# Kernel optimization log

Hardware: AMD Instinct MI355X
Metric: run time of the kernel (lower is better)

Reference implementation:

```python
import jax, jax.numpy as jnp
import numpy as np

N_NODES = 50000
N_EDGES = 1600000
IN_CH = 129   # encoding_dim + node_dim
OUT_CH = 64
PERIODS = 25
N_TRAIN = 25000


def setup_inputs() -> dict:
    key = jax.random.key(0)
    ks = jax.random.split(key, 24)
    inp = {
        'x': jax.random.normal(ks[0], (N_NODES, IN_CH, PERIODS), dtype=jnp.float32),
        'edge_index': jax.random.randint(ks[1], (2, N_EDGES), 0, N_NODES, dtype=jnp.int64),
        'y': jax.random.uniform(ks[2], (N_NODES,), dtype=jnp.float32),
        'train_idx': jax.random.randint(ks[3], (N_TRAIN,), 0, N_NODES, dtype=jnp.int64),
    }
    s_in = 1.0 / np.sqrt(IN_CH)
    s_2o = 1.0 / np.sqrt(2 * OUT_CH)
    s_o = 1.0 / np.sqrt(OUT_CH)
    # TGCN gate params: GCNConv weight/bias (IN_CH->OUT_CH), Linear(2*OUT_CH->OUT_CH)
    names = ['z', 'r', 'h']
    for i, g in enumerate(names):
        inp[f'W_{g}'] = jax.random.uniform(ks[4 + 4 * i], (IN_CH, OUT_CH), minval=-s_in, maxval=s_in)
        inp[f'b_{g}'] = jax.random.uniform(ks[5 + 4 * i], (OUT_CH,), minval=-s_in, maxval=s_in)
        inp[f'Wl_{g}'] = jax.random.uniform(ks[6 + 4 * i], (2 * OUT_CH, OUT_CH), minval=-s_2o, maxval=s_2o)
        inp[f'bl_{g}'] = jax.random.uniform(ks[7 + 4 * i], (OUT_CH,), minval=-s_2o, maxval=s_2o)
    inp['attention'] = jax.random.uniform(ks[16], (PERIODS,), dtype=jnp.float32)
    inp['W_o'] = jax.random.uniform(ks[17], (OUT_CH, 1), minval=-s_o, maxval=s_o)
    inp['b_o'] = jax.random.uniform(ks[18], (1,), minval=-s_o, maxval=s_o)
    return inp


def _forward(x, edge_index, y, train_idx, attention,
             W_z, b_z, Wl_z, bl_z, W_r, b_r, Wl_r, bl_r,
             W_h, b_h, Wl_h, bl_h, W_o, b_o):
    N = x.shape[0]
    src, dst = edge_index[0], edge_index[1]
    # GCN symmetric norm with self-loops (edge_weight = 1)
    deg = 1.0 + jax.ops.segment_sum(jnp.ones_like(src, dtype=x.dtype), dst, num_segments=N)
    dinv = jax.lax.rsqrt(deg)
    edge_norm = (dinv[src] * dinv[dst])[:, None]   # (E,1)
    self_norm = (dinv * dinv)[:, None]              # (N,1)

    def gcn(xt, W, b):
        h = xt @ W                                   # (N, OUT_CH)
        agg = jax.ops.segment_sum(edge_norm * h[src], dst, num_segments=N)
        return agg + self_norm * h + b

    probs = jax.nn.softmax(attention)               # (PERIODS,)
    x_seq = jnp.transpose(x, (2, 0, 1))             # (T, N, IN_CH)

    def step(carry, xp):
        H, acc = carry
        xt, p = xp
        Z = jax.nn.sigmoid(jnp.concatenate([gcn(xt, W_z, b_z), H], axis=1) @ Wl_z + bl_z)
        R = jax.nn.sigmoid(jnp.concatenate([gcn(xt, W_r, b_r), H], axis=1) @ Wl_r + bl_r)
        H_tilde = jnp.tanh(jnp.concatenate([gcn(xt, W_h, b_h), H * R], axis=1) @ Wl_h + bl_h)
        H = Z * H + (1.0 - Z) * H_tilde
        return (H, acc + p * H), None

    H0 = jnp.zeros((N, OUT_CH), dtype=x.dtype)
    (H, H_accum), _ = jax.lax.scan(step, (H0, H0), (x_seq, probs))

    out = jax.nn.sigmoid(H_accum @ W_o + b_o)       # (N, 1)
    y_pred = out[:, 0][train_idx]
    return y_pred, y[train_idx]


def reference(x, edge_index, y, train_idx, attention,
              W_z, b_z, Wl_z, bl_z, W_r, b_r, Wl_r, bl_r,
              W_h, b_h, Wl_h, bl_h, W_o, b_o):
    return _forward(x, edge_index, y, train_idx, attention,
                    W_z, b_z, Wl_z, bl_z, W_r, b_r, Wl_r, bl_r,
                    W_h, b_h, Wl_h, bl_h, W_o, b_o)
```

## Files before the change

### kernel.cpp

```cpp
#include <hip/hip_runtime.h>
#include <stdint.h>

#define NND 50000
#define NNDP 50016
#define NE  1600000
#define INC 129
#define TP  25
#define NTR 25000
#define MPAD 50048
#define NB_SCAN 196
#define CSR_MAX (NE + 8*NND + 128)
#define NFRAG 92
#define WLDS_BYTES (NFRAG*1024)

typedef short bf16x8 __attribute__((ext_vector_type(8)));
typedef float f32x4 __attribute__((ext_vector_type(4)));
typedef float f32x2 __attribute__((ext_vector_type(2)));
typedef uint32_t u32x4 __attribute__((ext_vector_type(4)));

__device__ __forceinline__ uint32_t f2bf(float f){
  union{float ff; uint32_t u;} v; v.ff=f;
  return (v.u + 0x7FFFu + ((v.u>>16)&1u))>>16;
}
__device__ __forceinline__ uint32_t pack2(float a, float b){
  return f2bf(a) | (f2bf(b)<<16);
}
__device__ __forceinline__ float sigm(float v){ return 1.f/(1.f+__expf(-v)); }

__global__ void k_prep(const float* Wz, const float* bz, const float* Wlz, const float* blz,
                       const float* Wr, const float* br, const float* Wlr, const float* blr,
                       const float* Wh, const float* bh, const float* Wlh, const float* blh,
                       uint16_t* WfT, uint16_t* Wlf)
{
  int idx = blockIdx.x*256 + threadIdx.x;
  if (idx < 192*224) {
    int j = idx / 224, k = idx - j*224;
    int g = j >> 6, jj = j & 63;
    const float* W  = g==0?Wz :(g==1?Wr :Wh);
    const float* Wl = g==0?Wlz:(g==1?Wlr:Wlh);
    const float* b  = g==0?bz :(g==1?br :bh);
    const float* bl = g==0?blz:(g==1?blr:blh);
    float v = 0.f;
    if (k < INC) {
      for (int m=0;m<64;m++) v += W[k*64+m]*Wl[m*64+jj];
    } else if (k == 129) {
      v = bl[jj];
      for (int m=0;m<64;m++) v += b[m]*Wl[m*64+jj];
    } else if (k >= 160) {
      v = (g<2) ? Wl[(64+(k-160))*64 + jj] : 0.f;
    }
    int rt = jj>>4, c16 = jj&15;
    int kk = k>>5, kgrp = (k>>3)&3, e = k&7;
    int lane = kgrp*16 + c16;
    WfT[((((g*7+kk)*4+rt)*256 + lane*4 + (e>>1))<<1) + (e&1)] = (uint16_t)f2bf(v);
  } else if (idx < 192*224 + 4096) {
    int t2 = idx - 192*224; int j2 = t2>>6, k2 = t2&63;
    float v = Wlh[(64+k2)*64 + j2];
    int rt = j2>>4, c16 = j2&15;
    int kk2 = k2>>5, kgrp = (k2>>3)&3, e = k2&7;
    int lane = kgrp*16 + c16;
    Wlf[(((kk2*4+rt)*256 + lane*4 + (e>>1))<<1) + (e&1)] = (uint16_t)f2bf(v);
  }
}

__global__ void k_probs(const float* att, float* probs){
  if (threadIdx.x==0 && blockIdx.x==0){
    float m=-1e30f;
    for (int i=0;i<TP;i++) m = fmaxf(m, att[i]);
    float e[TP]; float s=0.f;
    for (int i=0;i<TP;i++){ e[i]=__expf(att[i]-m); s+=e[i]; }
    for (int i=0;i<TP;i++) probs[i]=e[i]/s;
  }
}

__global__ void k_hist(const int* eidx, int* deg){
  int e = blockIdx.x*256 + threadIdx.x;
  if (e < NE) atomicAdd(&deg[eidx[NE + e]], 1);
}

__global__ void k_dinv(const int* deg, float* dinv){
  int n = blockIdx.x*256 + threadIdx.x;
  if (n < NND) dinv[n] = rsqrtf(1.0f + (float)deg[n]);
}

__global__ void k_scan1(const int* deg, int* row_ptr, int* bsum){
  __shared__ int s[256];
  int tid = threadIdx.x;
  int i = blockIdx.x*256 + tid;
  int v = (i < NND) ? ((deg[i]+8)&~7) : 0;
  s[tid] = v; __syncthreads();
  for (int d=1; d<256; d<<=1){
    int t = (tid>=d) ? s[tid-d] : 0;
    __syncthreads();
    s[tid] += t; __syncthreads();
  }
  if (i < NND) row_ptr[i] = s[tid] - v;
  if (tid == 255) bsum[blockIdx.x] = s[255];
}
__global__ void k_scan2(int* bsum, int* boff, int* row_ptr){
  __shared__ int s[256];
  int tid = threadIdx.x;
  int v = (tid < NB_SCAN) ? bsum[tid] : 0;
  s[tid] = v; __syncthreads();
  for (int d=1; d<256; d<<=1){
    int t = (tid>=d) ? s[tid-d] : 0;
    __syncthreads();
    s[tid] += t; __syncthreads();
  }
  if (tid < NB_SCAN) boff[tid] = s[tid] - v;
  if (tid == NB_SCAN-1) row_ptr[NND] = s[tid];
}
__global__ void k_scan3(int* row_ptr, const int* boff){
  int i = blockIdx.x*256 + threadIdx.x;
  if (i < NND) row_ptr[i] += boff[blockIdx.x];
}

__global__ void k_fill(const int* eidx, const int* rp, int* cnt, uint16_t* csr){
  int e = blockIdx.x*256 + threadIdx.x;
  if (e < NE){
    int s = eidx[e], d = eidx[NE+e];
    int pos = rp[d] + atomicAdd(&cnt[d],1);
    csr[pos] = (uint16_t)s;
  }
}
__global__ void k_self(const int* rp, const int* deg, uint16_t* csr){
  int n = blockIdx.x*256 + threadIdx.x;
  if (n < NND){
    int base = rp[n] + deg[n];
    int endp = rp[n+1];
    csr[base] = (uint16_t)n;
    for (int j=base+1; j<endp; j++) csr[j] = (uint16_t)NND;
  }
}

__global__ __launch_bounds__(256) void k_transpose3(const float* __restrict__ x,
                                                    const float* __restrict__ dinv,
                                                    uint32_t* __restrict__ xT8,
                                                    float* __restrict__ xsl){
  __shared__ float lx[3232];
  int n = blockIdx.x;
  const float* xr = x + (size_t)n*(INC*TP);
  for (int e=threadIdx.x; e<INC*TP; e+=256) lx[e] = xr[e];
  __syncthreads();
  float dv = dinv[n];
  for (int idx=threadIdx.x; idx<TP*32; idx+=256){
    int t = idx>>5, u = idx&31;
    int c0 = u*4;
    float v0 = lx[(c0+0)*TP+t]*dv, v1 = lx[(c0+1)*TP+t]*dv;
    float v2 = lx[(c0+2)*TP+t]*dv, v3 = lx[(c0+3)*TP+t]*dv;
    int wlo = __builtin_amdgcn_cvt_pk_fp8_f32(v0, v1, 0, false);
    int w   = __builtin_amdgcn_cvt_pk_fp8_f32(v2, v3, wlo, true);
    xT8[((size_t)t*NNDP + n)*32 + u] = (uint32_t)w;
  }
  for (int t=threadIdx.x; t<TP; t+=256)
    xsl[(size_t)t*NNDP + n] = dv*lx[128*TP + t];
  if (blockIdx.x == 0){
    for (int idx=threadIdx.x; idx<TP*32; idx+=256){
      int t = idx>>5, u = idx&31;
      xT8[((size_t)t*NNDP + NND)*32 + u] = 0u;
    }
    for (int t=threadIdx.x; t<TP; t+=256) xsl[(size_t)t*NNDP + NND] = 0.f;
  }
}

__global__ __launch_bounds__(256) void k_agg(const uint16_t* __restrict__ xT8,
    const int* __restrict__ rp, const uint16_t* __restrict__ csr,
    const float* __restrict__ dinv, uint32_t* __restrict__ AX)
{
  int t = blockIdx.y;
  int wave = threadIdx.x>>6, lane = threadIdx.x&63;
  int d = blockIdx.x*4 + wave;
  int beg = __builtin_amdgcn_readfirstlane(rp[d]);
  int end = __builtin_amdgcn_readfirstlane(rp[d+1]);
  const uint16_t* tbl = xT8 + (size_t)t*((size_t)NNDP*64);
  float a0=0.f, a1=0.f;
  for (int i0=beg; i0<end; i0+=8){
    ulonglong2 c = *(const ulonglong2*)(csr + i0);
    #pragma unroll
    for (int k=0;k<4;k++){
      int s0 = (int)((c.x >> (k*16)) & 0xFFFFu);
      int s1 = (int)((c.y >> (k*16)) & 0xFFFFu);
      uint32_t u0 = tbl[(size_t)s0*64 + lane];
      uint32_t u1 = tbl[(size_t)s1*64 + lane];
      f32x2 v0 = __builtin_amdgcn_cvt_pk_f32_fp8((int)u0, false);
      f32x2 v1 = __builtin_amdgcn_cvt_pk_f32_fp8((int)u1, false);
      a0 += v0.x; a1 += v0.y;
      a0 += v1.x; a1 += v1.y;
    }
  }
  float dv = dinv[d];
  AX[(size_t)t*((size_t)MPAD*80) + (size_t)d*80 + lane] = pack2(dv*a0, dv*a1);
}

__global__ void k_aggL(const float* __restrict__ xsl,
    const int* __restrict__ rp, const uint16_t* __restrict__ csr,
    const float* __restrict__ dinv, uint32_t* __restrict__ AX)
{
  int t = blockIdx.y;
  int d = blockIdx.x*256 + threadIdx.x;
  if (d >= NND) return;
  const float* pl = xsl + (size_t)t*NNDP;
  float a = 0.f;
  int beg=rp[d], end=rp[d+1];
  #pragma unroll 4
  for (int i=beg;i<end;i++) a += pl[(int)csr[i]];
  AX[(size_t)t*((size_t)MPAD*80) + (size_t)d*80 + 64] = pack2(dinv[d]*a, 1.0f);
}

__device__ __forceinline__ u32x4 build_frag(uint32_t Pa0, uint32_t Pa1,
                                            uint32_t Pb0, uint32_t Pb1,
                                            int srcA, int srcB, bool rsel){
  uint32_t a0 = (uint32_t)__shfl((int)Pa0, srcA);
  uint32_t b0 = (uint32_t)__shfl((int)Pb0, srcA);
  uint32_t a1 = (uint32_t)__shfl((int)Pa1, srcA);
  uint32_t b1 = (uint32_t)__shfl((int)Pb1, srcA);
  uint32_t a2 = (uint32_t)__shfl((int)Pa0, srcB);
  uint32_t b2 = (uint32_t)__shfl((int)Pb0, srcB);
  uint32_t a3 = (uint32_t)__shfl((int)Pa1, srcB);
  uint32_t b3 = (uint32_t)__shfl((int)Pb1, srcB);
  u32x4 o;
  o.x = rsel?b0:a0; o.y = rsel?b1:a1; o.z = rsel?b2:a2; o.w = rsel?b3:a3;
  return o;
}

__global__ __launch_bounds__(512, 2) void k_gru(const uint32_t* __restrict__ AX,
    const uint32_t* __restrict__ Wall, float* __restrict__ accum,
    const float* __restrict__ probs)
{
  extern __shared__ uint32_t ldsW[];
  int tid = threadIdx.x;
  int lane = tid & 63, wave = tid >> 6;
  int c16 = lane & 15, q = lane >> 4;
  int node = blockIdx.x*128 + wave*16 + c16;
  bool rsel = (q & 2) != 0;
  int srcA = ((2*q)&3)*16 + c16;
  int srcB = ((2*q+1)&3)*16 + c16;

  {
    const u32x4* src = (const u32x4*)Wall;
    u32x4* dst = (u32x4*)ldsW;
    for (int i = tid; i < NFRAG*64; i += 512) dst[i] = src[i];
  }
  __syncthreads();

  f32x4 h[4] = {};
  f32x4 acr[4] = {};
  u32x4 hf0 = {0,0,0,0}, hf1 = {0,0,0,0};

  for (int t=0; t<TP; t++){
    const uint32_t* AXrow = AX + (size_t)t*((size_t)MPAD*80) + (size_t)node*80 + q*4;
    bf16x8 ax0 = __builtin_nontemporal_load((const bf16x8*)(AXrow));
    bf16x8 ax1 = __builtin_nontemporal_load((const bf16x8*)(AXrow+16));
    bf16x8 ax2 = __builtin_nontemporal_load((const bf16x8*)(AXrow+32));
    bf16x8 ax3 = __builtin_nontemporal_load((const bf16x8*)(AXrow+48));
    bf16x8 ax4 = __builtin_nontemporal_load((const bf16x8*)(AXrow+64));

    f32x4 accg[3][4] = {};
    #pragma unroll
    for (int kk=0; kk<7; kk++){
      bf16x8 xv;
      if      (kk==0) xv = ax0;
      else if (kk==1) xv = ax1;
      else if (kk==2) xv = ax2;
      else if (kk==3) xv = ax3;
      else if (kk==4) xv = ax4;
      else if (kk==5) xv = __builtin_bit_cast(bf16x8, hf0);
      else            xv = __builtin_bit_cast(bf16x8, hf1);
      #pragma unroll
      for (int g=0; g<3; g++){
        if (g==2 && kk>=5) continue;
        #pragma unroll
        for (int rt=0; rt<4; rt++){
          bf16x8 wv = *(const bf16x8*)&ldsW[(((g*7+kk)*4+rt)<<8) + lane*4];
          accg[g][rt] = __builtin_amdgcn_mfma_f32_16x16x32_bf16(wv, xv, accg[g][rt],0,0,0);
        }
      }
    }

    uint32_t Phr[4][2];
    #pragma unroll
    for (int rt=0; rt<4; rt++){
      float hrv[4];
      #pragma unroll
      for (int j=0;j<4;j++){
        float z = sigm(accg[0][rt][j]);
        float r = sigm(accg[1][rt][j]);
        accg[0][rt][j] = z;
        hrv[j] = h[rt][j]*r;
      }
      Phr[rt][0] = pack2(hrv[0], hrv[1]);
      Phr[rt][1] = pack2(hrv[2], hrv[3]);
    }
    u32x4 hrf0 = build_frag(Phr[0][0],Phr[0][1],Phr[1][0],Phr[1][1], srcA,srcB,rsel);
    u32x4 hrf1 = build_frag(Phr[2][0],Phr[2][1],Phr[3][0],Phr[3][1], srcA,srcB,rsel);

    f32x4 acc2[4] = {};
    #pragma unroll
    for (int kk2=0; kk2<2; kk2++){
      bf16x8 bv = __builtin_bit_cast(bf16x8, kk2 ? hrf1 : hrf0);
      #pragma unroll
      for (int rt=0; rt<4; rt++){
        bf16x8 wv = *(const bf16x8*)&ldsW[((84+kk2*4+rt)<<8) + lane*4];
        acc2[rt] = __builtin_amdgcn_mfma_f32_16x16x32_bf16(wv, bv, acc2[rt],0,0,0);
      }
    }

    float pt = probs[t];
    uint32_t Ph[4][2];
    #pragma unroll
    for (int rt=0; rt<4; rt++){
      #pragma unroll
      for (int j=0;j<4;j++){
        float ht = tanhf(acc2[rt][j] + accg[2][rt][j]);
        float z  = accg[0][rt][j];
        float hn = z*h[rt][j] + (1.f-z)*ht;
        h[rt][j] = hn;
        acr[rt][j] += pt*hn;
      }
      Ph[rt][0] = pack2(h[rt][0], h[rt][1]);
      Ph[rt][1] = pack2(h[rt][2], h[rt][3]);
    }
    hf0 = build_frag(Ph[0][0],Ph[0][1],Ph[1][0],Ph[1][1], srcA,srcB,rsel);
    hf1 = build_frag(Ph[2][0],Ph[2][1],Ph[3][0],Ph[3][1], srcA,srcB,rsel);
  }

  if (node < NND){
    #pragma unroll
    for (int rt=0; rt<4; rt++)
      *(f32x4*)&accum[(size_t)node*64 + rt*16 + q*4] = acr[rt];
  }
}

__global__ void k_out(const int* train_idx, const float* accum, const float* Wo,
                      const float* bo, const float* y, float* out){
  int i = blockIdx.x*256 + threadIdx.x;
  if (i < NTR){
    int n = train_idx[i];
    float s = bo[0];
    const float* ar = accum + (size_t)n*64;
    #pragma unroll
    for (int j=0;j<64;j++) s += ar[j]*Wo[j];
    out[i] = sigm(s);
    out[NTR+i] = y[n];
  }
}

extern "C" void kernel_launch(void* const* d_in, const int* in_sizes, int n_in,
                              void* d_out, int out_size, void* d_ws, size_t ws_size,
                              hipStream_t stream)
{
  const float* x   = (const float*)d_in[0];
  const int*   eix = (const int*)d_in[1];
  const float* y   = (const float*)d_in[2];
  const int*   tri = (const int*)d_in[3];
  const float* Wz  = (const float*)d_in[4];
  const float* bz  = (const float*)d_in[5];
  const float* Wlz = (const float*)d_in[6];
  const float* blz = (const float*)d_in[7];
  const float* Wr  = (const float*)d_in[8];
  const float* br  = (const float*)d_in[9];
  const float* Wlr = (const float*)d_in[10];
  const float* blr = (const float*)d_in[11];
  const float* Wh  = (const float*)d_in[12];
  const float* bh  = (const float*)d_in[13];
  const float* Wlh = (const float*)d_in[14];
  const float* blh = (const float*)d_in[15];
  const float* att = (const float*)d_in[16];
  const float* Wo  = (const float*)d_in[17];
  const float* bo  = (const float*)d_in[18];
  float* out = (float*)d_out;

  char* w = (char*)d_ws;
  size_t off = 0;
  auto alloc = [&](size_t sz)->size_t{ size_t o=off; off=(off+sz+255)&~(size_t)255; return o; };

  size_t zo = off;
  size_t o_deg   = alloc((size_t)NND*4);
  size_t o_cnt   = alloc((size_t)NND*4);
  size_t zlen = off - zo;
  size_t o_dinv  = alloc((size_t)NND*4);
  size_t o_rp    = alloc((size_t)(NND+1)*4);
  size_t o_bsum  = alloc((size_t)NB_SCAN*4);
  size_t o_boff  = alloc((size_t)NB_SCAN*4);
  size_t o_csr   = alloc((size_t)CSR_MAX*2);
  size_t o_Wall  = alloc((size_t)NFRAG*1024);
  size_t o_probs = alloc((size_t)TP*4);
  size_t o_accum = alloc((size_t)MPAD*64*4);
  size_t o_AX    = alloc((size_t)TP*MPAD*80*4);
  size_t o_xT8   = alloc((size_t)TP*NNDP*128);
  size_t o_xl    = alloc((size_t)TP*NNDP*4);
  (void)ws_size; (void)in_sizes; (void)n_in; (void)out_size;

  int*      deg   = (int*)(w+o_deg);
  int*      cnt   = (int*)(w+o_cnt);
  float*    dinv  = (float*)(w+o_dinv);
  int*      rp    = (int*)(w+o_rp);
  int*      bsum  = (int*)(w+o_bsum);
  int*      boff  = (int*)(w+o_boff);
  uint16_t* csr   = (uint16_t*)(w+o_csr);
  uint16_t* WfT   = (uint16_t*)(w+o_Wall);
  uint16_t* Wlf   = WfT + 84*512;
  float*    probs = (float*)(w+o_probs);
  float*    accum = (float*)(w+o_accum);
  uint32_t* AX    = (uint32_t*)(w+o_AX);
  uint32_t* xT8   = (uint32_t*)(w+o_xT8);
  float*    xsl   = (float*)(w+o_xl);

  hipMemsetAsync(w+zo, 0, zlen, stream);

  k_prep<<<(192*224 + 4096 + 255)/256, 256, 0, stream>>>(
      Wz,bz,Wlz,blz, Wr,br,Wlr,blr, Wh,bh,Wlh,blh, WfT, Wlf);
  k_probs<<<1, 64, 0, stream>>>(att, probs);
  k_hist<<<(NE+255)/256, 256, 0, stream>>>(eix, deg);
  k_dinv<<<(NND+255)/256, 256, 0, stream>>>(deg, dinv);
  k_scan1<<<NB_SCAN, 256, 0, stream>>>(deg, rp, bsum);
  k_scan2<<<1, 256, 0, stream>>>(bsum, boff, rp);
  k_scan3<<<NB_SCAN, 256, 0, stream>>>(rp, boff);
  k_fill<<<(NE+255)/256, 256, 0, stream>>>(eix, rp, cnt, csr);
  k_self<<<NB_SCAN, 256, 0, stream>>>(rp, deg, csr);
  k_transpose3<<<NND, 256, 0, stream>>>(x, dinv, xT8, xsl);

  k_agg <<<dim3(12500, TP), 256, 0, stream>>>((const uint16_t*)xT8, rp, csr, dinv, AX);
  k_aggL<<<dim3(NB_SCAN, TP), 256, 0, stream>>>(xsl, rp, csr, dinv, AX);

  static bool attr_set = false;
  if (!attr_set){
    hipFuncSetAttribute((const void*)k_gru,
        hipFuncAttributeMaxDynamicSharedMemorySize, WLDS_BYTES);
    attr_set = true;
  }
  k_gru<<<MPAD/128, 512, WLDS_BYTES, stream>>>(AX, (const uint32_t*)WfT, accum, probs);
  k_out<<<(NTR+255)/256, 256, 0, stream>>>(tri, accum, Wo, bo, y, out);
}
```

Baseline: 2.258 ms.

## Split aggregated features into compact main and scalar buffers; restructure GRU gate GEMMs per gate

The aggregated activations move from a padded 80-word row per node to a 64-word bf16 block plus a separate float array for the extra 129th channel. This cuts the bytes written and read through the AX buffer. The GRU step now runs one GEMM per gate in sequence instead of interleaving all three accumulators, which lowers live register pressure and lets sigmoid work overlap later MFMAs. The nontemporal loads are dropped, and the LDS size attribute is now set on every call.

```diff
diff --git a/kernel.cpp b/kernel.cpp
--- a/kernel.cpp
+++ b/kernel.cpp
@@ -165,7 +165,7 @@
 
 __global__ __launch_bounds__(256) void k_agg(const uint16_t* __restrict__ xT8,
     const int* __restrict__ rp, const uint16_t* __restrict__ csr,
-    const float* __restrict__ dinv, uint32_t* __restrict__ AX)
+    const float* __restrict__ dinv, uint32_t* __restrict__ AX0)
 {
   int t = blockIdx.y;
   int wave = threadIdx.x>>6, lane = threadIdx.x&63;
@@ -189,12 +189,12 @@
     }
   }
   float dv = dinv[d];
-  AX[(size_t)t*((size_t)MPAD*80) + (size_t)d*80 + lane] = pack2(dv*a0, dv*a1);
+  AX0[((size_t)t*MPAD + d)*64 + lane] = pack2(dv*a0, dv*a1);
 }
 
 __global__ void k_aggL(const float* __restrict__ xsl,
     const int* __restrict__ rp, const uint16_t* __restrict__ csr,
-    const float* __restrict__ dinv, uint32_t* __restrict__ AX)
+    const float* __restrict__ dinv, float* __restrict__ AXL)
 {
   int t = blockIdx.y;
   int d = blockIdx.x*256 + threadIdx.x;
@@ -204,7 +204,7 @@
   int beg=rp[d], end=rp[d+1];
   #pragma unroll 4
   for (int i=beg;i<end;i++) a += pl[(int)csr[i]];
-  AX[(size_t)t*((size_t)MPAD*80) + (size_t)d*80 + 64] = pack2(dinv[d]*a, 1.0f);
+  AXL[(size_t)t*MPAD + d] = dinv[d]*a;
 }
 
 __device__ __forceinline__ u32x4 build_frag(uint32_t Pa0, uint32_t Pa1,
@@ -223,9 +223,26 @@
   return o;
 }
 
-__global__ __launch_bounds__(512, 2) void k_gru(const uint32_t* __restrict__ AX,
-    const uint32_t* __restrict__ Wall, float* __restrict__ accum,
-    const float* __restrict__ probs)
+template<int G, int KMAX>
+__device__ __forceinline__ void gate_gemm(const uint32_t* ldsW, int lane,
+    bf16x8 ax0, bf16x8 ax1, bf16x8 ax2, bf16x8 ax3, bf16x8 ax4,
+    u32x4 hf0, u32x4 hf1, f32x4* acc)
+{
+  #pragma unroll
+  for (int kk=0; kk<KMAX; kk++){
+    bf16x8 xv = (kk==0)?ax0:(kk==1)?ax1:(kk==2)?ax2:(kk==3)?ax3:(kk==4)?ax4:
+                (kk==5)?__builtin_bit_cast(bf16x8,hf0):__builtin_bit_cast(bf16x8,hf1);
+    #pragma unroll
+    for (int rt=0; rt<4; rt++){
+      bf16x8 wv = *(const bf16x8*)&ldsW[(((G*7+kk)*4+rt)<<8) + lane*4];
+      acc[rt] = __builtin_amdgcn_mfma_f32_16x16x32_bf16(wv, xv, acc[rt],0,0,0);
+    }
+  }
+}
+
+__global__ __launch_bounds__(512, 2) void k_gru(const uint32_t* __restrict__ AX0,
+    const float* __restrict__ AXL, const uint32_t* __restrict__ Wall,
+    float* __restrict__ accum, const float* __restrict__ probs)
 {
   extern __shared__ uint32_t ldsW[];
   int tid = threadIdx.x;
@@ -248,51 +265,40 @@
   u32x4 hf0 = {0,0,0,0}, hf1 = {0,0,0,0};
 
   for (int t=0; t<TP; t++){
-    const uint32_t* AXrow = AX + (size_t)t*((size_t)MPAD*80) + (size_t)node*80 + q*4;
-    bf16x8 ax0 = __builtin_nontemporal_load((const bf16x8*)(AXrow));
-    bf16x8 ax1 = __builtin_nontemporal_load((const bf16x8*)(AXrow+16));
-    bf16x8 ax2 = __builtin_nontemporal_load((const bf16x8*)(AXrow+32));
-    bf16x8 ax3 = __builtin_nontemporal_load((const bf16x8*)(AXrow+48));
-    bf16x8 ax4 = __builtin_nontemporal_load((const bf16x8*)(AXrow+64));
-
-    f32x4 accg[3][4] = {};
-    #pragma unroll
-    for (int kk=0; kk<7; kk++){
-      bf16x8 xv;
-      if      (kk==0) xv = ax0;
-      else if (kk==1) xv = ax1;
-      else if (kk==2) xv = ax2;
-      else if (kk==3) xv = ax3;
-      else if (kk==4) xv = ax4;
-      else if (kk==5) xv = __builtin_bit_cast(bf16x8, hf0);
-      else            xv = __builtin_bit_cast(bf16x8, hf1);
+    const uint32_t* AXrow = AX0 + ((size_t)t*MPAD + node)*64 + q*4;
+    bf16x8 ax0 = *(const bf16x8*)(AXrow);
+    bf16x8 ax1 = *(const bf16x8*)(AXrow+16);
+    bf16x8 ax2 = *(const bf16x8*)(AXrow+32);
+    bf16x8 ax3 = *(const bf16x8*)(AXrow+48);
+    float axl = AXL[(size_t)t*MPAD + node];
+    u32x4 x4u = {0,0,0,0};
+    if (q == 0) x4u.x = pack2(axl, 1.0f);
+    bf16x8 ax4 = __builtin_bit_cast(bf16x8, x4u);
+
+    f32x4 za[4] = {};
+    gate_gemm<0,7>(ldsW, lane, ax0,ax1,ax2,ax3,ax4, hf0, hf1, za);
+    #pragma unroll
+    for (int rt=0; rt<4; rt++)
       #pragma unroll
-      for (int g=0; g<3; g++){
-        if (g==2 && kk>=5) continue;
-        #pragma unroll
-        for (int rt=0; rt<4; rt++){
-          bf16x8 wv = *(const bf16x8*)&ldsW[(((g*7+kk)*4+rt)<<8) + lane*4];
-          accg[g][rt] = __builtin_amdgcn_mfma_f32_16x16x32_bf16(wv, xv, accg[g][rt],0,0,0);
-        }
-      }
-    }
-
+      for (int j=0;j<4;j++) za[rt][j] = sigm(za[rt][j]);
+
+    f32x4 ra[4] = {};
+    gate_gemm<1,7>(ldsW, lane, ax0,ax1,ax2,ax3,ax4, hf0, hf1, ra);
     uint32_t Phr[4][2];
     #pragma unroll
     for (int rt=0; rt<4; rt++){
-      float hrv[4];
-      #pragma unroll
-      for (int j=0;j<4;j++){
-        float z = sigm(accg[0][rt][j]);
-        float r = sigm(accg[1][rt][j]);
-        accg[0][rt][j] = z;
-        hrv[j] = h[rt][j]*r;
-      }
-      Phr[rt][0] = pack2(hrv[0], hrv[1]);
-      Phr[rt][1] = pack2(hrv[2], hrv[3]);
+      float hr0 = h[rt][0]*sigm(ra[rt][0]);
+      float hr1 = h[rt][1]*sigm(ra[rt][1]);
+      float hr2 = h[rt][2]*sigm(ra[rt][2]);
+      float hr3 = h[rt][3]*sigm(ra[rt][3]);
+      Phr[rt][0] = pack2(hr0, hr1);
+      Phr[rt][1] = pack2(hr2, hr3);
     }
     u32x4 hrf0 = build_frag(Phr[0][0],Phr[0][1],Phr[1][0],Phr[1][1], srcA,srcB,rsel);
     u32x4 hrf1 = build_frag(Phr[2][0],Phr[2][1],Phr[3][0],Phr[3][1], srcA,srcB,rsel);
+
+    f32x4 ph[4] = {};
+    gate_gemm<2,5>(ldsW, lane, ax0,ax1,ax2,ax3,ax4, hf0, hf1, ph);
 
     f32x4 acc2[4] = {};
     #pragma unroll
@@ -311,8 +317,8 @@
     for (int rt=0; rt<4; rt++){
       #pragma unroll
       for (int j=0;j<4;j++){
-        float ht = tanhf(acc2[rt][j] + accg[2][rt][j]);
-        float z  = accg[0][rt][j];
+        float ht = tanhf(acc2[rt][j] + ph[rt][j]);
+        float z  = za[rt][j];
         float hn = z*h[rt][j] + (1.f-z)*ht;
         h[rt][j] = hn;
         acr[rt][j] += pt*hn;
@@ -386,7 +392,8 @@
   size_t o_Wall  = alloc((size_t)NFRAG*1024);
   size_t o_probs = alloc((size_t)TP*4);
   size_t o_accum = alloc((size_t)MPAD*64*4);
-  size_t o_AX    = alloc((size_t)TP*MPAD*80*4);
+  size_t o_AX0   = alloc((size_t)TP*MPAD*256);
+  size_t o_AXL   = alloc((size_t)TP*MPAD*4);
   size_t o_xT8   = alloc((size_t)TP*NNDP*128);
   size_t o_xl    = alloc((size_t)TP*NNDP*4);
   (void)ws_size; (void)in_sizes; (void)n_in; (void)out_size;
@@ -402,7 +409,8 @@
   uint16_t* Wlf   = WfT + 84*512;
   float*    probs = (float*)(w+o_probs);
   float*    accum = (float*)(w+o_accum);
-  uint32_t* AX    = (uint32_t*)(w+o_AX);
+  uint32_t* AX0   = (uint32_t*)(w+o_AX0);
+  float*    AXL   = (float*)(w+o_AXL);
   uint32_t* xT8   = (uint32_t*)(w+o_xT8);
   float*    xsl   = (float*)(w+o_xl);
 
@@ -420,15 +428,12 @@
   k_self<<<NB_SCAN, 256, 0, stream>>>(rp, deg, csr);
   k_transpose3<<<NND, 256, 0, stream>>>(x, dinv, xT8, xsl);
 
-  k_agg <<<dim3(12500, TP), 256, 0, stream>>>((const uint16_t*)xT8, rp, csr, dinv, AX);
-  k_aggL<<<dim3(NB_SCAN, TP), 256, 0, stream>>>(xsl, rp, csr, dinv, AX);
-
-  static bool attr_set = false;
-  if (!attr_set){
-    hipFuncSetAttribute((const void*)k_gru,
-        hipFuncAttributeMaxDynamicSharedMemorySize, WLDS_BYTES);
-    attr_set = true;
-  }
-  k_gru<<<MPAD/128, 512, WLDS_BYTES, stream>>>(AX, (const uint32_t*)WfT, accum, probs);
+  k_agg <<<dim3(12500, TP), 256, 0, stream>>>((const uint16_t*)xT8, rp, csr, dinv, AX0);
+  k_aggL<<<dim3(NB_SCAN, TP), 256, 0, stream>>>(xsl, rp, csr, dinv, AXL);
+
+  hipFuncSetAttribute((const void*)k_gru,
+      hipFuncAttributeMaxDynamicSharedMemorySize, WLDS_BYTES);
+  k_gru<<<MPAD/128, 512, WLDS_BYTES, stream>>>(AX0, AXL, (const uint32_t*)WfT,
+                                               accum, probs);
   k_out<<<(NTR+255)/256, 256, 0, stream>>>(tri, accum, Wo, bo, y, out);
 }
```

After: 2.052 ms. 9.1% less time.
